# Kernel tuning notes

Measured on AMD Instinct MI355X. Metric: run time of the kernel, lower is better.

Reference implementation:

```python
import jax, jax.numpy as jnp
import numpy as np

D_MODEL = 1024
NUM_HEADS = 16
HEAD_DIM = D_MODEL // NUM_HEADS
BATCH, SEQ = 2, 2048


def setup_inputs() -> dict:
    key = jax.random.key(0)
    ks = jax.random.split(key, 5)
    scale = 1.0 / np.sqrt(D_MODEL)  # ~xavier magnitude
    x = jax.random.normal(ks[0], (BATCH, SEQ, D_MODEL), dtype=jnp.float32)
    Wq = jax.random.normal(ks[1], (D_MODEL, D_MODEL), dtype=jnp.float32) * scale
    Wk = jax.random.normal(ks[2], (D_MODEL, D_MODEL), dtype=jnp.float32) * scale
    Wv = jax.random.normal(ks[3], (D_MODEL, D_MODEL), dtype=jnp.float32) * scale
    Wo = jax.random.normal(ks[4], (D_MODEL, D_MODEL), dtype=jnp.float32) * scale
    z = jnp.zeros((D_MODEL,), dtype=jnp.float32)
    return {"x": x, "Wq": Wq, "bq": z, "Wk": Wk, "bk": z, "Wv": Wv, "bv": z, "Wo": Wo, "bo": z}


def reference(x, Wq, bq, Wk, bk, Wv, bv, Wo, bo):
    B, S, _ = x.shape
    H, Dh = NUM_HEADS, HEAD_DIM
    # torch Linear convention: y = x @ W^T + b
    q = (x @ Wq.T + bq).reshape(B, S, H, Dh)
    k = (x @ Wk.T + bk).reshape(B, S, H, Dh)
    v = (x @ Wv.T + bv).reshape(B, S, H, Dh)
    # scores: [B, H, S, S]
    scores = jnp.einsum('bqhd,bkhd->bhqk', q, k) / np.sqrt(Dh).astype(np.float32)
    attn = jax.nn.softmax(scores, axis=-1)
    out = jnp.einsum('bhqk,bkhd->bqhd', attn, v).reshape(B, S, H * Dh)
    return out @ Wo.T + bo
```

## Files before the change

### kernel.cpp

```cpp
#include <hip/hip_runtime.h>
#include <hip/hip_bf16.h>

typedef __bf16 bf16;
typedef __bf16 bf16x8 __attribute__((ext_vector_type(8)));
typedef __bf16 bf16x4 __attribute__((ext_vector_type(4)));
typedef float f32x4 __attribute__((ext_vector_type(4)));
typedef float f32x16 __attribute__((ext_vector_type(16)));
typedef unsigned int u32x4 __attribute__((ext_vector_type(4)));

constexpr int DM = 1024, NH = 16, DH = 64, NB = 2, SQ = 2048;
constexpr int MTOT = NB * SQ;
constexpr float QSCALE = 0.125f * 1.44269504088896f;

__device__ __forceinline__ void gld_lds16(const bf16* g, bf16* l) {
  __builtin_amdgcn_global_load_lds(
      (const __attribute__((address_space(1))) void*)g,
      (__attribute__((address_space(3))) void*)l, 16, 0, 0);
}

__global__ __launch_bounds__(256) void cvt5(
    const float* __restrict__ s0, const float* __restrict__ s1,
    const float* __restrict__ s2, const float* __restrict__ s3,
    const float* __restrict__ s4,
    bf16* __restrict__ d0, bf16* __restrict__ d1, bf16* __restrict__ d2,
    bf16* __restrict__ d3, bf16* __restrict__ d4) {
  const int idx = (blockIdx.x * 256 + threadIdx.x) * 8;
  const float* src; bf16* dst; int off;
  if (idx < 4 * DM * DM) {
    off = idx & (DM * DM - 1);
    switch (idx >> 20) {
      case 0: src = s0; dst = d0; break;
      case 1: src = s1; dst = d1; break;
      case 2: src = s2; dst = d2; break;
      default: src = s3; dst = d3; break;
    }
  } else {
    src = s4; dst = d4; off = idx - 4 * DM * DM;
  }
  const float4 a = *(const float4*)(src + off);
  const float4 b = *(const float4*)(src + off + 4);
  *(bf16x8*)(dst + off) = (bf16x8){(bf16)a.x, (bf16)a.y, (bf16)a.z, (bf16)a.w,
                                   (bf16)b.x, (bf16)b.y, (bf16)b.z, (bf16)b.w};
}

template <typename OutT>
__device__ __forceinline__ void gemm_tile128(
    const bf16* __restrict__ A, const bf16* __restrict__ Bm,
    const float* __restrict__ bias, OutT* __restrict__ C,
    int rowA0, int rowB0, int N, int K, bool bias_row, float cscale,
    bf16* sA, bf16* sB) {
  const int tid = threadIdx.x;
  const int wave = tid >> 6, lane = tid & 63;
  const int quad = lane >> 4, l16 = lane & 15;
  const int row0w = (wave >> 1) * 64;
  const int col0w = (wave & 1) * 64;

  f32x4 acc[4][4];
#pragma unroll
  for (int i = 0; i < 4; i++)
#pragma unroll
    for (int j = 0; j < 4; j++) acc[i][j] = (f32x4){0.f, 0.f, 0.f, 0.f};

  const int srow = lane >> 3;
  const int scol = ((lane & 7) ^ srow) * 8;

  for (int kt = 0; kt < K; kt += 64) {
#pragma unroll
    for (int i = 0; i < 4; i++) {
      const int r = i * 32 + wave * 8;
      gld_lds16(A + (size_t)(rowA0 + r + srow) * K + kt + scol, &sA[r * 64]);
      gld_lds16(Bm + (size_t)(rowB0 + r + srow) * K + kt + scol, &sB[r * 64]);
    }
    __syncthreads();
#pragma unroll
    for (int kk = 0; kk < 64; kk += 32) {
      bf16x8 aF[4], bF[4];
      const int slot = (((kk >> 3) + quad) ^ (l16 & 7)) << 3;
#pragma unroll
      for (int mt = 0; mt < 4; mt++)
        aF[mt] = *(const bf16x8*)&sA[(row0w + mt * 16 + l16) * 64 + slot];
#pragma unroll
      for (int nt = 0; nt < 4; nt++)
        bF[nt] = *(const bf16x8*)&sB[(col0w + nt * 16 + l16) * 64 + slot];
#pragma unroll
      for (int mt = 0; mt < 4; mt++)
#pragma unroll
        for (int nt = 0; nt < 4; nt++)
          acc[mt][nt] = __builtin_amdgcn_mfma_f32_16x16x32_bf16(aF[mt], bF[nt], acc[mt][nt], 0, 0, 0);
    }
    __syncthreads();
  }

#pragma unroll
  for (int mt = 0; mt < 4; mt++) {
#pragma unroll
    for (int nt = 0; nt < 4; nt++) {
#pragma unroll
      for (int r = 0; r < 4; r++) {
        const int row = rowA0 + row0w + mt * 16 + quad * 4 + r;
        const int col = rowB0 + col0w + nt * 16 + l16;
        const float bb = bias_row ? bias[row] : bias[col];
        C[(size_t)row * N + col] = (OutT)((acc[mt][nt][r] + bb) * cscale);
      }
    }
  }
}

__global__ __launch_bounds__(256, 4) void qkv_gemm(
    const bf16* __restrict__ xb, const bf16* __restrict__ Wqb,
    const bf16* __restrict__ Wkb, const bf16* __restrict__ Wvb,
    const float* __restrict__ bq, const float* __restrict__ bk,
    const float* __restrict__ bv,
    bf16* __restrict__ Qw, bf16* __restrict__ Kw, bf16* __restrict__ VTw) {
  __shared__ alignas(16) bf16 sA[128 * 64];
  __shared__ alignas(16) bf16 sB[128 * 64];
  if (blockIdx.z == 0) {
    gemm_tile128<bf16>(xb, Wqb, bq, Qw, blockIdx.x * 128, blockIdx.y * 128, DM, DM, false, QSCALE, sA, sB);
  } else if (blockIdx.z == 1) {
    gemm_tile128<bf16>(xb, Wkb, bk, Kw, blockIdx.x * 128, blockIdx.y * 128, DM, DM, false, 1.0f, sA, sB);
  } else {
    const int id = blockIdx.y * 32 + blockIdx.x;
    gemm_tile128<bf16>(Wvb, xb, bv, VTw, (id >> 5) * 128, (id & 31) * 128, MTOT, DM, true, 1.0f, sA, sB);
  }
}

__global__ __launch_bounds__(256, 3) void out_gemm(
    const bf16* __restrict__ A, const bf16* __restrict__ Bm,
    const float* __restrict__ bias, float* __restrict__ C) {
  __shared__ alignas(16) bf16 sA[2][64 * 64];
  __shared__ alignas(16) bf16 sB[2][128 * 64];
  const int tid = threadIdx.x;
  const int wave = tid >> 6, lane = tid & 63;
  const int quad = lane >> 4, l16 = lane & 15;
  const int col0w = wave * 32;
  const int rowA0 = blockIdx.x * 64, rowB0 = blockIdx.y * 128;

  f32x4 acc[4][2];
#pragma unroll
  for (int i = 0; i < 4; i++)
#pragma unroll
    for (int j = 0; j < 2; j++) acc[i][j] = (f32x4){0.f, 0.f, 0.f, 0.f};

  const int srow = lane >> 3;
  const int scol = ((lane & 7) ^ srow) * 8;

  auto stage = [&](int kt, int buf) {
#pragma unroll
    for (int i = 0; i < 2; i++) {
      const int r = i * 32 + wave * 8;
      gld_lds16(A + (size_t)(rowA0 + r + srow) * DM + kt * 64 + scol, &sA[buf][r * 64]);
    }
#pragma unroll
    for (int i = 0; i < 4; i++) {
      const int r = i * 32 + wave * 8;
      gld_lds16(Bm + (size_t)(rowB0 + r + srow) * DM + kt * 64 + scol, &sB[buf][r * 64]);
    }
  };

  stage(0, 0);
  for (int t = 0; t < 16; ++t) {
    __syncthreads();
    if (t + 1 < 16) stage(t + 1, (t + 1) & 1);
    const bf16* cA = sA[t & 1];
    const bf16* cB = sB[t & 1];
#pragma unroll
    for (int kk = 0; kk < 64; kk += 32) {
      bf16x8 aF[4], bF[2];
      const int slot = (((kk >> 3) + quad) ^ (l16 & 7)) << 3;
#pragma unroll
      for (int mt = 0; mt < 4; mt++)
        aF[mt] = *(const bf16x8*)&cA[(mt * 16 + l16) * 64 + slot];
#pragma unroll
      for (int nt = 0; nt < 2; nt++)
        bF[nt] = *(const bf16x8*)&cB[(col0w + nt * 16 + l16) * 64 + slot];
#pragma unroll
      for (int mt = 0; mt < 4; mt++)
#pragma unroll
        for (int nt = 0; nt < 2; nt++)
          acc[mt][nt] = __builtin_amdgcn_mfma_f32_16x16x32_bf16(aF[mt], bF[nt], acc[mt][nt], 0, 0, 0);
    }
  }

#pragma unroll
  for (int mt = 0; mt < 4; mt++) {
#pragma unroll
    for (int nt = 0; nt < 2; nt++) {
#pragma unroll
      for (int r = 0; r < 4; r++) {
        const int row = rowA0 + mt * 16 + quad * 4 + r;
        const int col = rowB0 + col0w + nt * 16 + l16;
        C[(size_t)row * DM + col] = acc[mt][nt][r] + bias[col];
      }
    }
  }
}

__global__ __launch_bounds__(256, 2) void attn(
    const bf16* __restrict__ Q, const bf16* __restrict__ Kq,
    const bf16* __restrict__ VT, bf16* __restrict__ O) {
  __shared__ alignas(16) bf16 sK[2][64 * 64];
  __shared__ alignas(16) bf16 sV[2][64 * 64];
  const int tid = threadIdx.x, wave = tid >> 6, lane = tid & 63;
  const int l32 = lane & 31, half = lane >> 5;
  const int hb = blockIdx.x, qt = blockIdx.y;
  const int h = hb & 15, b = hb >> 4;

  const bf16* Qg = Q + (size_t)(b * SQ + qt * 128 + wave * 32) * DM + h * DH;
  const bf16* Kg = Kq + (size_t)(b * SQ) * DM + h * DH;
  const bf16* Vg = VT + (size_t)(h * DH) * MTOT + b * SQ;

  const int srow = lane >> 3, scol = ((lane & 7) ^ srow) * 8;

  auto stageKV = [&](int t, int buf) {
#pragma unroll
    for (int i = 0; i < 2; i++) {
      const int r = (wave * 2 + i) * 8;
      gld_lds16(Kg + (size_t)(t * 64 + r + srow) * DM + scol, &sK[buf][r * 64]);
      gld_lds16(Vg + (size_t)(r + srow) * MTOT + t * 64 + scol, &sV[buf][r * 64]);
    }
  };

  bf16x8 qF[4];
#pragma unroll
  for (int kk = 0; kk < 4; kk++)
    qF[kk] = *(const bf16x8*)(Qg + (size_t)l32 * DM + kk * 16 + half * 8);

  f32x16 o_acc[2];
#pragma unroll
  for (int nd = 0; nd < 2; nd++)
#pragma unroll
    for (int i = 0; i < 16; i++) o_acc[nd][i] = 0.f;
  f32x4 lsum4 = (f32x4){0.f, 0.f, 0.f, 0.f};

  stageKV(0, 0);
  for (int t = 0; t < 32; ++t) {
    __syncthreads();
    if (t + 1 < 32) stageKV(t + 1, (t + 1) & 1);
    const bf16* cK = sK[t & 1];
    const bf16* cV = sV[t & 1];
    const int sw7 = l32 & 7;

    f32x16 sacc[2];
#pragma unroll
    for (int nt = 0; nt < 2; nt++)
#pragma unroll
      for (int i = 0; i < 16; i++) sacc[nt][i] = 0.f;

    bf16x8 kf[2][4];
#pragma unroll
    for (int nt = 0; nt < 2; nt++)
#pragma unroll
      for (int kk = 0; kk < 4; kk++)
        kf[nt][kk] = *(const bf16x8*)&cK[(nt * 32 + l32) * 64 + (((kk * 2 + half) ^ sw7) << 3)];
    __builtin_amdgcn_s_setprio(1);
#pragma unroll
    for (int nt = 0; nt < 2; nt++)
#pragma unroll
      for (int kk = 0; kk < 4; kk++)
        sacc[nt] = __builtin_amdgcn_mfma_f32_32x32x16_bf16(kf[nt][kk], qF[kk], sacc[nt], 0, 0, 0);
    __builtin_amdgcn_s_setprio(0);

#pragma unroll
    for (int nt = 0; nt < 2; nt++) {
      float p[16];
#pragma unroll
      for (int i = 0; i < 16; i++) {
        p[i] = __builtin_amdgcn_exp2f(sacc[nt][i]);
        lsum4[i & 3] += p[i];
      }
      unsigned int w[8];
#pragma unroll
      for (int i = 0; i < 8; i++)
        asm("v_cvt_pk_bf16_f32 %0, %1, %2" : "=v"(w[i]) : "v"(p[2 * i]), "v"(p[2 * i + 1]));
      asm("v_permlane32_swap_b32 %0, %1" : "+v"(w[0]), "+v"(w[2]));
      asm("v_permlane32_swap_b32 %0, %1" : "+v"(w[1]), "+v"(w[3]));
      asm("v_permlane32_swap_b32 %0, %1" : "+v"(w[4]), "+v"(w[6]));
      asm("v_permlane32_swap_b32 %0, %1" : "+v"(w[5]), "+v"(w[7]));
#pragma unroll
      for (int s = 0; s < 2; s++) {
        const u32x4 pw = (s == 0) ? (u32x4){w[0], w[1], w[2], w[3]}
                                  : (u32x4){w[4], w[5], w[6], w[7]};
        const bf16x8 pb = __builtin_bit_cast(bf16x8, pw);
        const int ks = nt * 2 + s;
        bf16x8 vf[2];
#pragma unroll
        for (int nd = 0; nd < 2; nd++)
          vf[nd] = *(const bf16x8*)&cV[(nd * 32 + l32) * 64 + (((ks * 2 + half) ^ sw7) << 3)];
        __builtin_amdgcn_s_setprio(1);
#pragma unroll
        for (int nd = 0; nd < 2; nd++)
          o_acc[nd] = __builtin_amdgcn_mfma_f32_32x32x16_bf16(vf[nd], pb, o_acc[nd], 0, 0, 0);
        __builtin_amdgcn_s_setprio(0);
      }
    }
  }

  const float lsum = (lsum4[0] + lsum4[1]) + (lsum4[2] + lsum4[3]);
  const float lother = __shfl(lsum, lane ^ 32, 64);
  const float inv = 1.0f / (lsum + lother);

  bf16* Op = O + (size_t)(b * SQ + qt * 128 + wave * 32 + l32) * DM + h * DH;
#pragma unroll
  for (int nd = 0; nd < 2; nd++) {
#pragma unroll
    for (int g = 0; g < 4; g++) {
      bf16x4 ov;
#pragma unroll
      for (int r = 0; r < 4; r++) ov[r] = (bf16)(o_acc[nd][g * 4 + r] * inv);
      *(bf16x4*)(Op + nd * 32 + g * 8 + half * 4) = ov;
    }
  }
}

extern "C" void kernel_launch(void* const* d_in, const int* in_sizes, int n_in,
                              void* d_out, int out_size, void* d_ws, size_t ws_size,
                              hipStream_t stream) {
  const float* x  = (const float*)d_in[0];
  const float* Wq = (const float*)d_in[1];
  const float* bq = (const float*)d_in[2];
  const float* Wk = (const float*)d_in[3];
  const float* bk = (const float*)d_in[4];
  const float* Wv = (const float*)d_in[5];
  const float* bv = (const float*)d_in[6];
  const float* Wo = (const float*)d_in[7];
  const float* bo = (const float*)d_in[8];
  float* out = (float*)d_out;

  bf16* ws   = (bf16*)d_ws;
  bf16* xb   = ws;
  bf16* Wqb  = ws + (size_t)MTOT * DM;
  bf16* Wkb  = Wqb + (size_t)DM * DM;
  bf16* Wvb  = Wkb + (size_t)DM * DM;
  bf16* Wob  = Wvb + (size_t)DM * DM;
  bf16* Qw   = Wob + (size_t)DM * DM;
  bf16* Kw   = Qw + (size_t)MTOT * DM;
  bf16* VTw  = Kw + (size_t)MTOT * DM;
  bf16* Cw   = VTw + (size_t)MTOT * DM;

  const dim3 blk(256);
  cvt5<<<dim3((4 * DM * DM + MTOT * DM) / 2048, 1), blk, 0, stream>>>(
      Wq, Wk, Wv, Wo, x, Wqb, Wkb, Wvb, Wob, xb);
  qkv_gemm<<<dim3(32, 8, 3), blk, 0, stream>>>(xb, Wqb, Wkb, Wvb, bq, bk, bv, Qw, Kw, VTw);
  attn<<<dim3(NH * NB, SQ / 128), blk, 0, stream>>>(Qw, Kw, VTw, Cw);
  out_gemm<<<dim3(MTOT / 64, DM / 128), blk, 0, stream>>>(Cw, Wob, bo, out);
}
```

Before: 180.3 us.

## Software-pipeline attention PV matmul one tile behind QK with triple-buffered LDS

Restructures the attention loop so the P·V MFMAs for tile t-1 are issued alongside the QK^T MFMAs of tile t, letting the exp/softmax conversion overlap with matrix work. K/V LDS buffers go from double to triple buffering so the previous V tile stays resident, and an epilogue finishes the last PV step. This raises LDS use (48KB per block) and register pressure from the held P fragments and eight V fragments, which may affect occupancy at 2 blocks per CU.

```diff
diff --git a/kernel.cpp b/kernel.cpp
--- a/kernel.cpp
+++ b/kernel.cpp
@@ -198,8 +198,8 @@
 __global__ __launch_bounds__(256, 2) void attn(
     const bf16* __restrict__ Q, const bf16* __restrict__ Kq,
     const bf16* __restrict__ VT, bf16* __restrict__ O) {
-  __shared__ alignas(16) bf16 sK[2][64 * 64];
-  __shared__ alignas(16) bf16 sV[2][64 * 64];
+  __shared__ alignas(16) bf16 sK[3][64 * 64];
+  __shared__ alignas(16) bf16 sV[3][64 * 64];
   const int tid = threadIdx.x, wave = tid >> 6, lane = tid & 63;
   const int l32 = lane & 31, half = lane >> 5;
   const int hb = blockIdx.x, qt = blockIdx.y;
@@ -231,28 +231,46 @@
 #pragma unroll
     for (int i = 0; i < 16; i++) o_acc[nd][i] = 0.f;
   f32x4 lsum4 = (f32x4){0.f, 0.f, 0.f, 0.f};
+  bf16x8 pbPrev[4];
+
+  const int sw7 = l32 & 7;
 
   stageKV(0, 0);
   for (int t = 0; t < 32; ++t) {
     __syncthreads();
-    if (t + 1 < 32) stageKV(t + 1, (t + 1) & 1);
-    const bf16* cK = sK[t & 1];
-    const bf16* cV = sV[t & 1];
-    const int sw7 = l32 & 7;
-
-    f32x16 sacc[2];
-#pragma unroll
-    for (int nt = 0; nt < 2; nt++)
-#pragma unroll
-      for (int i = 0; i < 16; i++) sacc[nt][i] = 0.f;
-
+    if (t + 1 < 32) stageKV(t + 1, (t + 1) % 3);
+    const bf16* cK = sK[t % 3];
+    const bf16* cVp = sV[(t + 2) % 3];
+
+    bf16x8 vf[4][2];
+    if (t > 0) {
+#pragma unroll
+      for (int ks = 0; ks < 4; ks++)
+#pragma unroll
+        for (int nd = 0; nd < 2; nd++)
+          vf[ks][nd] = *(const bf16x8*)&cVp[(nd * 32 + l32) * 64 + (((ks * 2 + half) ^ sw7) << 3)];
+    }
     bf16x8 kf[2][4];
 #pragma unroll
     for (int nt = 0; nt < 2; nt++)
 #pragma unroll
       for (int kk = 0; kk < 4; kk++)
         kf[nt][kk] = *(const bf16x8*)&cK[(nt * 32 + l32) * 64 + (((kk * 2 + half) ^ sw7) << 3)];
+
+    f32x16 sacc[2];
+#pragma unroll
+    for (int nt = 0; nt < 2; nt++)
+#pragma unroll
+      for (int i = 0; i < 16; i++) sacc[nt][i] = 0.f;
+
     __builtin_amdgcn_s_setprio(1);
+    if (t > 0) {
+#pragma unroll
+      for (int ks = 0; ks < 4; ks++)
+#pragma unroll
+        for (int nd = 0; nd < 2; nd++)
+          o_acc[nd] = __builtin_amdgcn_mfma_f32_32x32x16_bf16(vf[ks][nd], pbPrev[ks], o_acc[nd], 0, 0, 0);
+    }
 #pragma unroll
     for (int nt = 0; nt < 2; nt++)
 #pragma unroll
@@ -276,21 +294,19 @@
       asm("v_permlane32_swap_b32 %0, %1" : "+v"(w[1]), "+v"(w[3]));
       asm("v_permlane32_swap_b32 %0, %1" : "+v"(w[4]), "+v"(w[6]));
       asm("v_permlane32_swap_b32 %0, %1" : "+v"(w[5]), "+v"(w[7]));
-#pragma unroll
-      for (int s = 0; s < 2; s++) {
-        const u32x4 pw = (s == 0) ? (u32x4){w[0], w[1], w[2], w[3]}
-                                  : (u32x4){w[4], w[5], w[6], w[7]};
-        const bf16x8 pb = __builtin_bit_cast(bf16x8, pw);
-        const int ks = nt * 2 + s;
-        bf16x8 vf[2];
-#pragma unroll
-        for (int nd = 0; nd < 2; nd++)
-          vf[nd] = *(const bf16x8*)&cV[(nd * 32 + l32) * 64 + (((ks * 2 + half) ^ sw7) << 3)];
-        __builtin_amdgcn_s_setprio(1);
-#pragma unroll
-        for (int nd = 0; nd < 2; nd++)
-          o_acc[nd] = __builtin_amdgcn_mfma_f32_32x32x16_bf16(vf[nd], pb, o_acc[nd], 0, 0, 0);
-        __builtin_amdgcn_s_setprio(0);
+      pbPrev[nt * 2 + 0] = __builtin_bit_cast(bf16x8, (u32x4){w[0], w[1], w[2], w[3]});
+      pbPrev[nt * 2 + 1] = __builtin_bit_cast(bf16x8, (u32x4){w[4], w[5], w[6], w[7]});
+    }
+  }
+
+  {
+    const bf16* cVp = sV[31 % 3];
+#pragma unroll
+    for (int ks = 0; ks < 4; ks++) {
+#pragma unroll
+      for (int nd = 0; nd < 2; nd++) {
+        const bf16x8 vfe = *(const bf16x8*)&cVp[(nd * 32 + l32) * 64 + (((ks * 2 + half) ^ sw7) << 3)];
+        o_acc[nd] = __builtin_amdgcn_mfma_f32_32x32x16_bf16(vfe, pbPrev[ks], o_acc[nd], 0, 0, 0);
       }
     }
   }
```

After: 184.5 us. +2.4%, slower.
